# Kernel optimization log

Measured on AMD Instinct MI355X. Metric: run time of the kernel, lower is better.

## Reference

```python
import jax, jax.numpy as jnp
import numpy as np

B, S, D = 8, 4096, 512
EPS = 1e-6


def setup_inputs() -> dict:
    key = jax.random.key(0)
    ks = jax.random.split(key, 9)
    scale = 1.0 / np.sqrt(D)
    inp = {
        "x_seq": jax.random.normal(ks[0], (B, S, D), dtype=jnp.float32),
        "Wq": jax.random.uniform(ks[1], (D, D), jnp.float32, -scale, scale),
        "bq": jax.random.uniform(ks[2], (D,), jnp.float32, -scale, scale),
        "Wk": jax.random.uniform(ks[3], (D, D), jnp.float32, -scale, scale),
        "bk": jax.random.uniform(ks[4], (D,), jnp.float32, -scale, scale),
        "Wv": jax.random.uniform(ks[5], (D, D), jnp.float32, -scale, scale),
        "bv": jax.random.uniform(ks[6], (D,), jnp.float32, -scale, scale),
        "Wa": jax.random.uniform(ks[7], (D, D), jnp.float32, -scale, scale),
        "ba": jax.random.uniform(ks[8], (D,), jnp.float32, -scale, scale),
    }
    return inp


def _forward(x_seq, Wq, bq, Wk, bk, Wv, bv, Wa, ba):
    # Precompute all projections for the whole sequence (big GEMMs).
    q = jax.nn.relu(jnp.einsum('bsd,ed->bse', x_seq, Wq) + bq)  # phi = relu
    k = jax.nn.relu(jnp.einsum('bsd,ed->bse', x_seq, Wk) + bk)
    v = jnp.einsum('bsd,ed->bse', x_seq, Wv) + bv
    a = jax.nn.sigmoid(jnp.einsum('bsd,ed->bse', x_seq, Wa) + ba)

    # time-major for scan: (S, B, D)
    qs, ks_, vs, as_ = (jnp.swapaxes(t, 0, 1) for t in (q, k, v, a))

    def step(carry, inp):
        s, z = carry                      # s: (B,D,D), z: (B,D)
        q_t, k_t, v_t, a_t = inp
        s = a_t[:, :, None] * s + k_t[:, :, None] * v_t[:, None, :]
        z = a_t * z + k_t
        num = jnp.einsum('bi,bij->bj', q_t, s)
        den = jnp.sum(q_t * z, axis=-1, keepdims=True) + EPS
        return (s, z), num / den

    s0 = jnp.zeros((x_seq.shape[0], x_seq.shape[2], x_seq.shape[2]), x_seq.dtype)
    z0 = jnp.zeros((x_seq.shape[0], x_seq.shape[2]), x_seq.dtype)
    _, ys = jax.lax.scan(step, (s0, z0), (qs, ks_, vs, as_))
    return jnp.swapaxes(ys, 0, 1)  # (B, S, D)


def reference(x_seq, Wq, bq, Wk, bk, Wv, bv, Wa, ba):
    return _forward(x_seq, Wq, bq, Wk, bk, Wv, bv, Wa, ba)
```

## Files before the change

### kernel.cpp

```cpp
#include <hip/hip_runtime.h>
#include <hip/hip_bf16.h>
#include <cstdint>
#include <cstddef>

#define D_DIM 512
#define B_DIM 8
#define S_DIM 4096
#define M_DIM (B_DIM * S_DIM)
#define CHUNK 64
#define NCHUNK (S_DIM / CHUNK)
#define NSEG 8
#define CSEG (NCHUNK / NSEG)
#define EPS_C 1e-6f

typedef __attribute__((ext_vector_type(8))) short bf16x8;
typedef __attribute__((ext_vector_type(4))) float f32x4;

#define GLOAD_LDS16(src, dst)                                              \
  __builtin_amdgcn_global_load_lds(                                        \
      (const __attribute__((address_space(1))) void*)(src),                \
      (__attribute__((address_space(3))) void*)(dst), 16, 0, 0)

__device__ __forceinline__ unsigned short f2bf(float f) {
  uint32_t u = __float_as_uint(f);
  u = (u + 0x7fffu + ((u >> 16) & 1u)) >> 16;
  return (unsigned short)u;
}
__device__ __forceinline__ float bf2f(unsigned short s) { return __uint_as_float(((uint32_t)s) << 16); }

__global__ void cvt_f32_bf16(const float* __restrict__ in, unsigned short* __restrict__ out, int n4) {
  int i = blockIdx.x * blockDim.x + threadIdx.x;
  int stride = gridDim.x * blockDim.x;
  for (; i < n4; i += stride) {
    float4 f = ((const float4*)in)[i];
    ushort4 o;
    o.x = f2bf(f.x); o.y = f2bf(f.y); o.z = f2bf(f.z); o.w = f2bf(f.w);
    ((ushort4*)out)[i] = o;
  }
}

#define PTM 256
#define PTN 256
#define PBK 64

__global__ __launch_bounds__(512, 2) void proj_gemm(
    const unsigned short* __restrict__ Xb,
    const unsigned short* __restrict__ Wb,
    const float* __restrict__ bq, const float* __restrict__ bk,
    const float* __restrict__ bv, const float* __restrict__ ba,
    unsigned short* __restrict__ q_ws, unsigned short* __restrict__ k_ws,
    unsigned short* __restrict__ v_ws, unsigned short* __restrict__ g_ws) {
  __shared__ unsigned short SB[2 * (PTM + PTN) * PBK];

  const int proj = blockIdx.z;
  const unsigned short* W = Wb + (size_t)proj * D_DIM * D_DIM;
  const int m0 = blockIdx.x * PTM;
  const int n0 = blockIdx.y * PTN;
  const int lane = threadIdx.x & 63;
  const int w = threadIdx.x >> 6;
  const int l16 = lane & 15, q4 = lane >> 4;
  const int wm = (w >> 2) * 128;
  const int wn = (w & 3) * 64;

  f32x4 acc[8][4];
#pragma unroll
  for (int m = 0; m < 8; ++m)
#pragma unroll
    for (int n = 0; n < 4; ++n) acc[m][n] = (f32x4){0.f, 0.f, 0.f, 0.f};

  const int srow = lane >> 3;
  const int sg = lane & 7;

  auto STAGE = [&](int buf, int kc) {
    unsigned short* A = SB + buf * ((PTM + PTN) * PBK);
    unsigned short* Bs = A + PTM * PBK;
#pragma unroll
    for (int q = 0; q < 4; ++q) {
      const int row = w * 32 + q * 8 + srow;
      const int g = sg ^ (row & 7);
      GLOAD_LDS16(&Xb[(size_t)(m0 + row) * D_DIM + kc + g * 8], &A[(w * 32 + q * 8) * PBK]);
      GLOAD_LDS16(&W[(size_t)(n0 + row) * D_DIM + kc + g * 8], &Bs[(w * 32 + q * 8) * PBK]);
    }
  };

  STAGE(0, 0);
  __syncthreads();

  for (int t = 0; t < D_DIM / PBK; ++t) {
    const int cur = t & 1;
    if (t + 1 < D_DIM / PBK) STAGE(cur ^ 1, (t + 1) * PBK);

    const unsigned short* A = SB + cur * ((PTM + PTN) * PBK);
    const unsigned short* Bs = A + PTM * PBK;
    const int rsw = l16 & 7;
#pragma unroll
    for (int ks = 0; ks < 2; ++ks) {
      const int gphys = ((ks * 4 + q4) ^ rsw) * 8;
      bf16x8 afr[8], bfr[4];
#pragma unroll
      for (int m = 0; m < 8; ++m)
        afr[m] = *(const bf16x8*)&A[(wm + m * 16 + l16) * PBK + gphys];
#pragma unroll
      for (int n = 0; n < 4; ++n)
        bfr[n] = *(const bf16x8*)&Bs[(wn + n * 16 + l16) * PBK + gphys];
#pragma unroll
      for (int m = 0; m < 8; ++m)
#pragma unroll
        for (int n = 0; n < 4; ++n)
          acc[m][n] = __builtin_amdgcn_mfma_f32_16x16x32_bf16(afr[m], bfr[n], acc[m][n], 0, 0, 0);
    }
    __syncthreads();
  }

  const float* bias = (proj == 0) ? bq : (proj == 1) ? bk : (proj == 2) ? bv : ba;
  unsigned short* outp = (proj == 0) ? q_ws : (proj == 1) ? k_ws : (proj == 2) ? v_ws : g_ws;
  const bool do_relu = (proj <= 1);
  unsigned short* EP = &SB[w * 128 * 32];

#pragma unroll
  for (int p = 0; p < 2; ++p) {
#pragma unroll
    for (int half = 0; half < 2; ++half) {
      const int in_idx = p * 2 + half;
      const int nn = n0 + wn + in_idx * 16 + l16;
      const float bn = bias[nn];
#pragma unroll
      for (int m = 0; m < 8; ++m) {
#pragma unroll
        for (int vv = 0; vv < 4; ++vv) {
          float val = acc[m][in_idx][vv] + bn;
          if (do_relu) val = fmaxf(val, 0.f);
          EP[(m * 16 + q4 * 4 + vv) * 32 + half * 16 + l16] = f2bf(val);
        }
      }
    }
#pragma unroll
    for (int it = 0; it < 8; ++it) {
      const int row = it * 16 + (lane >> 2);
      const int ccol = (lane & 3) * 8;
      bf16x8 vdat = *(const bf16x8*)&EP[row * 32 + ccol];
      size_t gidx = (size_t)(m0 + wm + row) * D_DIM + (size_t)(n0 + wn + p * 32 + ccol);
      *(bf16x8*)&outp[gidx] = vdat;
    }
  }
}

__global__ __launch_bounds__(512) void prep(
    const unsigned short* __restrict__ q, const unsigned short* __restrict__ k,
    const unsigned short* __restrict__ g,
    unsigned short* __restrict__ qt, unsigned short* __restrict__ kt,
    unsigned short* __restrict__ kh,
    float* __restrict__ Af, float* __restrict__ khs) {
  __shared__ float segp[8][512];
  const int c = blockIdx.x, b = blockIdx.y;
  const int seg = threadIdx.x >> 6;
  const int t = threadIdx.x & 63;
  const int i0 = t * 8;
  const int r0 = seg * 8;
  const size_t t0 = (size_t)b * S_DIM + (size_t)c * CHUNK;
  const size_t cb = ((size_t)b * NCHUNK + c) * D_DIM;

  float sp[8];
#pragma unroll
  for (int j = 0; j < 8; ++j) sp[j] = 1.f;
  for (int r = 0; r < 8; ++r) {
    bf16x8 gv = *(const bf16x8*)&g[(t0 + r0 + r) * D_DIM + i0];
#pragma unroll
    for (int j = 0; j < 8; ++j)
      sp[j] *= 1.f / (1.f + __expf(-bf2f((unsigned short)gv[j])));
  }
  *(float4*)&segp[seg][i0] = *(float4*)&sp[0];
  *(float4*)&segp[seg][i0 + 4] = *(float4*)&sp[4];
  __syncthreads();

  float pre[8], tot[8];
#pragma unroll
  for (int j = 0; j < 8; ++j) { pre[j] = 1.f; tot[j] = 1.f; }
  for (int s2 = 0; s2 < 8; ++s2) {
    float4 v0 = *(const float4*)&segp[s2][i0];
    float4 v1 = *(const float4*)&segp[s2][i0 + 4];
    float v[8] = {v0.x, v0.y, v0.z, v0.w, v1.x, v1.y, v1.z, v1.w};
#pragma unroll
    for (int j = 0; j < 8; ++j) {
      tot[j] *= v[j];
      if (s2 < seg) pre[j] *= v[j];
    }
  }
  if (seg == 0) {
    float4 a0 = {tot[0], tot[1], tot[2], tot[3]};
    float4 a1 = {tot[4], tot[5], tot[6], tot[7]};
    *(float4*)&Af[cb + i0] = a0;
    *(float4*)&Af[cb + i0 + 4] = a1;
  }

  float cum[8], ssum[8];
#pragma unroll
  for (int j = 0; j < 8; ++j) { cum[j] = pre[j]; ssum[j] = 0.f; }
  for (int r = 0; r < 8; ++r) {
    size_t idx = (t0 + r0 + r) * D_DIM + i0;
    bf16x8 gv = *(const bf16x8*)&g[idx];
    bf16x8 qv8 = *(const bf16x8*)&q[idx];
    bf16x8 kv8 = *(const bf16x8*)&k[idx];
    bf16x8 oq, ok, okh;
#pragma unroll
    for (int j = 0; j < 8; ++j) {
      cum[j] *= 1.f / (1.f + __expf(-bf2f((unsigned short)gv[j])));
      float qv = bf2f((unsigned short)qv8[j]);
      float kv = bf2f((unsigned short)kv8[j]);
      oq[j] = (short)f2bf(qv * cum[j]);
      float inv = 1.f / cum[j];
      ok[j] = (short)f2bf(kv * inv);
      float khf = kv * (tot[j] * inv);
      okh[j] = (short)f2bf(khf);
      ssum[j] += khf;
    }
    *(bf16x8*)&qt[idx] = oq;
    *(bf16x8*)&kt[idx] = ok;
    *(bf16x8*)&kh[idx] = okh;
  }

  __syncthreads();
  *(float4*)&segp[seg][i0] = *(float4*)&ssum[0];
  *(float4*)&segp[seg][i0 + 4] = *(float4*)&ssum[4];
  __syncthreads();
  if (seg == 0) {
    float s[8];
#pragma unroll
    for (int j = 0; j < 8; ++j) s[j] = 0.f;
    for (int s2 = 0; s2 < 8; ++s2) {
      float4 v0 = *(const float4*)&segp[s2][i0];
      float4 v1 = *(const float4*)&segp[s2][i0 + 4];
      s[0] += v0.x; s[1] += v0.y; s[2] += v0.z; s[3] += v0.w;
      s[4] += v1.x; s[5] += v1.y; s[6] += v1.z; s[7] += v1.w;
    }
    float4 a0 = {s[0], s[1], s[2], s[3]};
    float4 a1 = {s[4], s[5], s[6], s[7]};
    *(float4*)&khs[cb + i0] = a0;
    *(float4*)&khs[cb + i0 + 4] = a1;
  }
}

__global__ __launch_bounds__(256) void transpose_cd(
    const unsigned short* __restrict__ in, unsigned short* __restrict__ outT) {
  __shared__ unsigned short tile[CHUNK][264];
  const int c = blockIdx.x, b = blockIdx.y;
  const size_t base_in = ((size_t)b * S_DIM + (size_t)c * CHUNK) * D_DIM;
  const size_t base_out = ((size_t)b * NCHUNK + c) * (size_t)D_DIM * CHUNK;
  const int tid = threadIdx.x;
#pragma unroll
  for (int h = 0; h < 2; ++h) {
    if (h) __syncthreads();
#pragma unroll
    for (int it = 0; it < 8; ++it) {
      int flat = (it * 256 + tid) * 8;
      int row = flat >> 8;
      int col = flat & 255;
      *(uint4*)&tile[row][col] = *(const uint4*)&in[base_in + (size_t)row * D_DIM + h * 256 + col];
    }
    __syncthreads();
#pragma unroll
    for (int it = 0; it < 8; ++it) {
      int wq = it * 256 + tid;
      int i_loc = wq >> 3;
      int r0 = (wq & 7) * 8;
      ushort4 v0, v1;
      v0.x = tile[r0 + 0][i_loc]; v0.y = tile[r0 + 1][i_loc];
      v0.z = tile[r0 + 2][i_loc]; v0.w = tile[r0 + 3][i_loc];
      v1.x = tile[r0 + 4][i_loc]; v1.y = tile[r0 + 5][i_loc];
      v1.z = tile[r0 + 6][i_loc]; v1.w = tile[r0 + 7][i_loc];
      size_t o = base_out + (size_t)(h * 256 + i_loc) * CHUNK + r0;
      *(ushort4*)&outT[o] = v0;
      *(ushort4*)&outT[o + 4] = v1;
    }
  }
}

__global__ __launch_bounds__(256) void intra(
    const unsigned short* __restrict__ qt, const unsigned short* kt,
    const unsigned short* __restrict__ VT,
    unsigned short* numI, float* __restrict__ rs) {
  __shared__ unsigned short P_lds[CHUNK][CHUNK + 8];
  const int c = blockIdx.x, b = blockIdx.y;
  const size_t t0 = (size_t)b * S_DIM + (size_t)c * CHUNK;
  const int lane = threadIdx.x & 63, w = threadIdx.x >> 6;
  const int l16 = lane & 15, q4 = lane >> 4;

  f32x4 accP[4];
#pragma unroll
  for (int n = 0; n < 4; ++n) accP[n] = (f32x4){0.f, 0.f, 0.f, 0.f};
#pragma unroll
  for (int ks = 0; ks < 16; ++ks) {
    bf16x8 afr = *(const bf16x8*)&qt[(t0 + 16 * w + l16) * D_DIM + 32 * ks + 8 * q4];
#pragma unroll
    for (int n = 0; n < 4; ++n) {
      bf16x8 bfr = *(const bf16x8*)&kt[(t0 + 16 * n + l16) * D_DIM + 32 * ks + 8 * q4];
      accP[n] = __builtin_amdgcn_mfma_f32_16x16x32_bf16(afr, bfr, accP[n], 0, 0, 0);
    }
  }
  float rsum[4] = {0.f, 0.f, 0.f, 0.f};
#pragma unroll
  for (int n = 0; n < 4; ++n) {
    int m = 16 * n + l16;
#pragma unroll
    for (int vv = 0; vv < 4; ++vv) {
      int r = 16 * w + 4 * q4 + vv;
      float pv = (m <= r) ? accP[n][vv] : 0.f;
      rsum[vv] += pv;
      P_lds[r][m] = f2bf(pv);
    }
  }
#pragma unroll
  for (int msk = 1; msk < 16; msk <<= 1) {
#pragma unroll
    for (int vv = 0; vv < 4; ++vv) rsum[vv] += __shfl_xor(rsum[vv], msk, 64);
  }
  if (l16 == 0) {
#pragma unroll
    for (int vv = 0; vv < 4; ++vv) rs[t0 + 16 * w + 4 * q4 + vv] = rsum[vv];
  }
  __syncthreads();
  bf16x8 pa0 = *(const bf16x8*)&P_lds[16 * w + l16][8 * q4];
  bf16x8 pa1 = *(const bf16x8*)&P_lds[16 * w + l16][32 + 8 * q4];
  const size_t vtb = ((size_t)b * NCHUNK + c) * (size_t)D_DIM * CHUNK;
#pragma unroll 4
  for (int nt = 0; nt < 32; ++nt) {
    bf16x8 b0 = *(const bf16x8*)&VT[vtb + (size_t)(nt * 16 + l16) * CHUNK + 8 * q4];
    bf16x8 b1 = *(const bf16x8*)&VT[vtb + (size_t)(nt * 16 + l16) * CHUNK + 32 + 8 * q4];
    f32x4 acc = (f32x4){0.f, 0.f, 0.f, 0.f};
    acc = __builtin_amdgcn_mfma_f32_16x16x32_bf16(pa0, b0, acc, 0, 0, 0);
    acc = __builtin_amdgcn_mfma_f32_16x16x32_bf16(pa1, b1, acc, 0, 0, 0);
#pragma unroll
    for (int vv = 0; vv < 4; ++vv)
      numI[(t0 + 16 * w + 4 * q4 + vv) * D_DIM + nt * 16 + l16] = f2bf(acc[vv]);
  }
}

__global__ __launch_bounds__(512) void zscan(
    const float* __restrict__ Af, const float* __restrict__ khs,
    float* __restrict__ zall, float* __restrict__ Pseg) {
  const int b = blockIdx.x;
  const int i = threadIdx.x;
  float z = 0.f, rp = 1.f;
  for (int c = 0; c < NCHUNK; ++c) {
    const size_t cb = ((size_t)b * NCHUNK + c) * D_DIM;
    zall[cb + i] = z;
    float af = Af[cb + i];
    z = fmaf(af, z, khs[cb + i]);
    rp *= af;
    if ((c & (CSEG - 1)) == CSEG - 1) {
      Pseg[((size_t)b * NSEG + (c / CSEG)) * D_DIM + i] = rp;
      rp = 1.f;
    }
  }
}

__global__ __launch_bounds__(512) void denk(
    const unsigned short* __restrict__ qt, const float* __restrict__ zall,
    float* rs_invden) {
  const int c = blockIdx.x, b = blockIdx.y;
  const int lane = threadIdx.x & 63, w = threadIdx.x >> 6;
  const size_t t0 = (size_t)b * S_DIM + (size_t)c * CHUNK;
  const size_t zb = ((size_t)b * NCHUNK + c) * D_DIM;
  float4 z0 = *(const float4*)&zall[zb + lane * 8];
  float4 z1 = *(const float4*)&zall[zb + lane * 8 + 4];
#pragma unroll
  for (int rr = 0; rr < 8; ++rr) {
    int r = 8 * w + rr;
    bf16x8 qv = *(const bf16x8*)&qt[(t0 + r) * D_DIM + lane * 8];
    float p = 0.f;
    p = fmaf(bf2f((unsigned short)qv[0]), z0.x, p);
    p = fmaf(bf2f((unsigned short)qv[1]), z0.y, p);
    p = fmaf(bf2f((unsigned short)qv[2]), z0.z, p);
    p = fmaf(bf2f((unsigned short)qv[3]), z0.w, p);
    p = fmaf(bf2f((unsigned short)qv[4]), z1.x, p);
    p = fmaf(bf2f((unsigned short)qv[5]), z1.y, p);
    p = fmaf(bf2f((unsigned short)qv[6]), z1.z, p);
    p = fmaf(bf2f((unsigned short)qv[7]), z1.w, p);
#pragma unroll
    for (int msk = 1; msk < 64; msk <<= 1) p += __shfl_xor(p, msk, 64);
    if (lane == 0) {
      float* iv = &rs_invden[t0 + r];
      *iv = 1.f / (p + *iv + EPS_C);
    }
  }
}

__global__ __launch_bounds__(512, 2) void useg_k(
    const unsigned short* __restrict__ khT, const unsigned short* __restrict__ VT,
    const float* __restrict__ Af, unsigned short* __restrict__ U) {
  __shared__ unsigned short VTl[2][128 * 64];
  const int s = blockIdx.x, jt = blockIdx.y, b = blockIdx.z;
  const int lane = threadIdx.x & 63, w = threadIdx.x >> 6;
  const int l16 = lane & 15, q4 = lane >> 4;
  const int j0 = jt * 128;
  const int iw = 64 * w;
  const int vrow = lane >> 3;
  const int vswz = (lane & 7) ^ (vrow & 7);

  f32x4 acc[4][8];
#pragma unroll
  for (int T = 0; T < 4; ++T)
#pragma unroll
    for (int h = 0; h < 8; ++h) acc[T][h] = (f32x4){0.f, 0.f, 0.f, 0.f};

  const size_t cb0 = ((size_t)b * NCHUNK + s * CSEG) * D_DIM;
  {
    const size_t ob0 = cb0 * CHUNK;
#pragma unroll
    for (int kk = 0; kk < 2; ++kk) {
      const int k = 2 * w + kk;
      GLOAD_LDS16(&VT[ob0 + (size_t)(j0 + 8 * k + vrow) * CHUNK + vswz * 8],
                  &VTl[0][k * 512]);
    }
  }
  bf16x8 a0[4], a1[4];
  {
    const size_t ob0 = cb0 * CHUNK;
#pragma unroll
    for (int T = 0; T < 4; ++T) {
      a0[T] = *(const bf16x8*)&khT[ob0 + (size_t)(iw + 16 * T + l16) * CHUNK + 8 * q4];
      a1[T] = *(const bf16x8*)&khT[ob0 + (size_t)(iw + 16 * T + l16) * CHUNK + 32 + 8 * q4];
    }
  }

  for (int cc = 0; cc < CSEG; ++cc) {
    const size_t cb = cb0 + (size_t)cc * D_DIM;
    __syncthreads();
    if (cc + 1 < CSEG) {
      const size_t obn = (cb + D_DIM) * CHUNK;
#pragma unroll
      for (int kk = 0; kk < 2; ++kk) {
        const int k = 2 * w + kk;
        GLOAD_LDS16(&VT[obn + (size_t)(j0 + 8 * k + vrow) * CHUNK + vswz * 8],
                    &VTl[(cc + 1) & 1][k * 512]);
      }
    }
#pragma unroll
    for (int T = 0; T < 4; ++T) {
      float4 af = *(const float4*)&Af[cb + iw + 16 * T + 4 * q4];
#pragma unroll
      for (int h = 0; h < 8; ++h) {
        acc[T][h][0] *= af.x; acc[T][h][1] *= af.y; acc[T][h][2] *= af.z; acc[T][h][3] *= af.w;
      }
    }
    const unsigned short* Vb = VTl[cc & 1];
#pragma unroll
    for (int h = 0; h < 8; ++h) {
      const int jpos = 16 * h + l16;
      const int swz = jpos & 7;
      bf16x8 bv0 = *(const bf16x8*)&Vb[jpos * 64 + ((q4 ^ swz) * 8)];
      bf16x8 bv1 = *(const bf16x8*)&Vb[jpos * 64 + (((4 + q4) ^ swz) * 8)];
#pragma unroll
      for (int T = 0; T < 4; ++T) {
        acc[T][h] = __builtin_amdgcn_mfma_f32_16x16x32_bf16(a0[T], bv0, acc[T][h], 0, 0, 0);
        acc[T][h] = __builtin_amdgcn_mfma_f32_16x16x32_bf16(a1[T], bv1, acc[T][h], 0, 0, 0);
      }
    }
    if (cc + 1 < CSEG) {
      const size_t obn = (cb + D_DIM) * CHUNK;
#pragma unroll
      for (int T = 0; T < 4; ++T) {
        a0[T] = *(const bf16x8*)&khT[obn + (size_t)(iw + 16 * T + l16) * CHUNK + 8 * q4];
        a1[T] = *(const bf16x8*)&khT[obn + (size_t)(iw + 16 * T + l16) * CHUNK + 32 + 8 * q4];
      }
    }
  }
  const size_t ub = ((size_t)b * NSEG + s) * D_DIM;
#pragma unroll
  for (int T = 0; T < 4; ++T)
#pragma unroll
    for (int h = 0; h < 8; ++h) {
      uint2 pk;
      pk.x = (uint32_t)f2bf(acc[T][h][0]) | ((uint32_t)f2bf(acc[T][h][1]) << 16);
      pk.y = (uint32_t)f2bf(acc[T][h][2]) | ((uint32_t)f2bf(acc[T][h][3]) << 16);
      *(uint2*)&U[(ub + j0 + 16 * h + l16) * (size_t)D_DIM + iw + 16 * T + 4 * q4] = pk;
    }
}

__global__ __launch_bounds__(256) void sscan(
    const float* __restrict__ Pseg, unsigned short* __restrict__ U) {
  const int b = blockIdx.y;
  const int flat = blockIdx.x * 256 + threadIdx.x;
  const int j = flat >> 6;
  const int i0 = (flat & 63) * 8;
  float acc[8];
#pragma unroll
  for (int t = 0; t < 8; ++t) acc[t] = 0.f;
  for (int s = 0; s < NSEG; ++s) {
    const size_t pb = ((size_t)b * NSEG + s) * D_DIM;
    unsigned short* up = &U[(pb + j) * (size_t)D_DIM + i0];
    uint4 u = *(const uint4*)up;
    float4 p0 = *(const float4*)&Pseg[pb + i0];
    float4 p1 = *(const float4*)&Pseg[pb + i0 + 4];
    float uv[8];
    uv[0] = bf2f((unsigned short)(u.x & 0xffff)); uv[1] = bf2f((unsigned short)(u.x >> 16));
    uv[2] = bf2f((unsigned short)(u.y & 0xffff)); uv[3] = bf2f((unsigned short)(u.y >> 16));
    uv[4] = bf2f((unsigned short)(u.z & 0xffff)); uv[5] = bf2f((unsigned short)(u.z >> 16));
    uv[6] = bf2f((unsigned short)(u.w & 0xffff)); uv[7] = bf2f((unsigned short)(u.w >> 16));
    uint4 o;
    o.x = (uint32_t)f2bf(acc[0]) | ((uint32_t)f2bf(acc[1]) << 16);
    o.y = (uint32_t)f2bf(acc[2]) | ((uint32_t)f2bf(acc[3]) << 16);
    o.z = (uint32_t)f2bf(acc[4]) | ((uint32_t)f2bf(acc[5]) << 16);
    o.w = (uint32_t)f2bf(acc[6]) | ((uint32_t)f2bf(acc[7]) << 16);
    *(uint4*)up = o;
    acc[0] = fmaf(p0.x, acc[0], uv[0]);
    acc[1] = fmaf(p0.y, acc[1], uv[1]);
    acc[2] = fmaf(p0.z, acc[2], uv[2]);
    acc[3] = fmaf(p0.w, acc[3], uv[3]);
    acc[4] = fmaf(p1.x, acc[4], uv[4]);
    acc[5] = fmaf(p1.y, acc[5], uv[5]);
    acc[6] = fmaf(p1.z, acc[6], uv[6]);
    acc[7] = fmaf(p1.w, acc[7], uv[7]);
  }
}

__global__ __launch_bounds__(512, 2) void scan2(
    const unsigned short* __restrict__ qt, const unsigned short* __restrict__ khT,
    const unsigned short* __restrict__ VT, const float* __restrict__ Af,
    const unsigned short* __restrict__ Sin,
    const unsigned short* __restrict__ numI, const float* __restrict__ invden,
    float* __restrict__ out) {
  __shared__ unsigned short STj[128][520];
  __shared__ unsigned short VTl[128 * 64];
  const int s = blockIdx.x, jt = blockIdx.y, b = blockIdx.z;
  const int lane = threadIdx.x & 63, w = threadIdx.x >> 6;
  const int l16 = lane & 15, q4 = lane >> 4;
  const int j0 = jt * 128;
  const int iw = 64 * w;
  const int rw = 16 * (w & 3);
  const int jo = 64 * (w >> 2);
  const int vrow = lane >> 3;
  const int vswz = (lane & 7) ^ (vrow & 7);

  f32x4 acc[4][8];

  {
    const size_t pb = ((size_t)b * NSEG + s) * D_DIM;
#pragma unroll
    for (int T = 0; T < 4; ++T)
#pragma unroll
      for (int h = 0; h < 8; ++h) {
        uint2 uu = *(const uint2*)&Sin[(pb + j0 + 16 * h + l16) * (size_t)D_DIM + iw + 16 * T + 4 * q4];
        acc[T][h][0] = bf2f((unsigned short)(uu.x & 0xffff));
        acc[T][h][1] = bf2f((unsigned short)(uu.x >> 16));
        acc[T][h][2] = bf2f((unsigned short)(uu.y & 0xffff));
        acc[T][h][3] = bf2f((unsigned short)(uu.y >> 16));
      }
  }

  for (int cc = 0; cc < CSEG; ++cc) {
    const int c = s * CSEG + cc;
    const size_t cb = ((size_t)b * NCHUNK + c) * D_DIM;
    const size_t t0 = (size_t)b * S_DIM + (size_t)c * CHUNK;
    const size_t ob = cb * CHUNK;
    const bool upd = (cc != CSEG - 1);

    bf16x8 a0[4], a1[4];
    if (upd) {
#pragma unroll
      for (int kk = 0; kk < 2; ++kk) {
        const int k = 2 * w + kk;
        GLOAD_LDS16(&VT[ob + (size_t)(j0 + 8 * k + vrow) * CHUNK + vswz * 8],
                    &VTl[k * 512]);
      }
#pragma unroll
      for (int T = 0; T < 4; ++T) {
        a0[T] = *(const bf16x8*)&khT[ob + (size_t)(iw + 16 * T + l16) * CHUNK + 8 * q4];
        a1[T] = *(const bf16x8*)&khT[ob + (size_t)(iw + 16 * T + l16) * CHUNK + 32 + 8 * q4];
      }
    }

#pragma unroll
    for (int T = 0; T < 4; ++T)
#pragma unroll
      for (int h = 0; h < 8; ++h) {
        uint2 pk;
        pk.x = (uint32_t)f2bf(acc[T][h][0]) | ((uint32_t)f2bf(acc[T][h][1]) << 16);
        pk.y = (uint32_t)f2bf(acc[T][h][2]) | ((uint32_t)f2bf(acc[T][h][3]) << 16);
        *(uint2*)&STj[16 * h + l16][iw + 16 * T + 4 * q4] = pk;
      }
    __syncthreads();

    {
      f32x4 accO[4];
#pragma unroll
      for (int h = 0; h < 4; ++h) accO[h] = (f32x4){0.f, 0.f, 0.f, 0.f};
#pragma unroll
      for (int ks = 0; ks < 16; ++ks) {
        bf16x8 afr = *(const bf16x8*)&qt[(t0 + rw + l16) * D_DIM + 32 * ks + 8 * q4];
#pragma unroll
        for (int h = 0; h < 4; ++h) {
          bf16x8 bfr = *(const bf16x8*)&STj[jo + 16 * h + l16][32 * ks + 8 * q4];
          accO[h] = __builtin_amdgcn_mfma_f32_16x16x32_bf16(afr, bfr, accO[h], 0, 0, 0);
        }
      }
#pragma unroll
      for (int h = 0; h < 4; ++h)
#pragma unroll
        for (int vv = 0; vv < 4; ++vv) {
          size_t t = t0 + rw + 4 * q4 + vv;
          int j = j0 + jo + 16 * h + l16;
          float idv = invden[t];
          float nI = bf2f(numI[t * D_DIM + j]);
          out[t * D_DIM + j] = (accO[h][vv] + nI) * idv;
        }
    }

    if (upd) {
#pragma unroll
      for (int T = 0; T < 4; ++T) {
        float4 af = *(const float4*)&Af[cb + iw + 16 * T + 4 * q4];
#pragma unroll
        for (int h = 0; h < 8; ++h) {
          acc[T][h][0] *= af.x; acc[T][h][1] *= af.y; acc[T][h][2] *= af.z; acc[T][h][3] *= af.w;
        }
      }
#pragma unroll
      for (int h = 0; h < 8; ++h) {
        const int jpos = 16 * h + l16;
        const int swz = jpos & 7;
        bf16x8 bv0 = *(const bf16x8*)&VTl[jpos * 64 + ((q4 ^ swz) * 8)];
        bf16x8 bv1 = *(const bf16x8*)&VTl[jpos * 64 + (((4 + q4) ^ swz) * 8)];
#pragma unroll
        for (int T = 0; T < 4; ++T) {
          acc[T][h] = __builtin_amdgcn_mfma_f32_16x16x32_bf16(a0[T], bv0, acc[T][h], 0, 0, 0);
          acc[T][h] = __builtin_amdgcn_mfma_f32_16x16x32_bf16(a1[T], bv1, acc[T][h], 0, 0, 0);
        }
      }
    }
    __syncthreads();
  }
}

extern "C" void kernel_launch(void* const* d_in, const int* in_sizes, int n_in,
                              void* d_out, int out_size, void* d_ws, size_t ws_size,
                              hipStream_t stream) {
  const float* x  = (const float*)d_in[0];
  const float* Wq = (const float*)d_in[1];
  const float* bq = (const float*)d_in[2];
  const float* Wk = (const float*)d_in[3];
  const float* bk = (const float*)d_in[4];
  const float* Wv = (const float*)d_in[5];
  const float* bv = (const float*)d_in[6];
  const float* Wa = (const float*)d_in[7];
  const float* ba = (const float*)d_in[8];
  float* out = (float*)d_out;

  const size_t MD2 = (size_t)M_DIM * D_DIM * 2;
  uint8_t* w = (uint8_t*)d_ws;
  unsigned short* xb   = (unsigned short*)w; w += MD2;
  unsigned short* wb   = (unsigned short*)w; w += (size_t)4 * D_DIM * D_DIM * 2;
  unsigned short* q_ws = (unsigned short*)w; w += MD2;
  unsigned short* k_ws = (unsigned short*)w; w += MD2;
  unsigned short* v_ws = (unsigned short*)w; w += MD2;
  unsigned short* g_ws = (unsigned short*)w; w += MD2;
  float* Af     = (float*)w; w += (size_t)B_DIM * NCHUNK * D_DIM * 4;
  float* khs    = (float*)w; w += (size_t)B_DIM * NCHUNK * D_DIM * 4;
  float* invden = (float*)w; w += (size_t)M_DIM * 4;

  unsigned short* qt   = xb;
  unsigned short* kt   = q_ws;
  unsigned short* kh   = k_ws;
  unsigned short* VT   = g_ws;
  unsigned short* khT  = v_ws;
  unsigned short* numI = q_ws;
  unsigned short* U    = k_ws;
  float* zall = (float*)wb;
  float* Pseg = (float*)((uint8_t*)wb + (1 << 20));

  cvt_f32_bf16<<<1024, 256, 0, stream>>>(x, xb, M_DIM * D_DIM / 4);
  cvt_f32_bf16<<<128, 256, 0, stream>>>(Wq, wb + 0 * D_DIM * D_DIM, D_DIM * D_DIM / 4);
  cvt_f32_bf16<<<128, 256, 0, stream>>>(Wk, wb + 1 * D_DIM * D_DIM, D_DIM * D_DIM / 4);
  cvt_f32_bf16<<<128, 256, 0, stream>>>(Wv, wb + 2 * D_DIM * D_DIM, D_DIM * D_DIM / 4);
  cvt_f32_bf16<<<128, 256, 0, stream>>>(Wa, wb + 3 * D_DIM * D_DIM, D_DIM * D_DIM / 4);

  proj_gemm<<<dim3(M_DIM / PTM, D_DIM / PTN, 4), 512, 0, stream>>>(
      xb, wb, bq, bk, bv, ba, q_ws, k_ws, v_ws, g_ws);

  prep<<<dim3(NCHUNK, B_DIM), 512, 0, stream>>>(q_ws, k_ws, g_ws, qt, kt, kh, Af, khs);
  transpose_cd<<<dim3(NCHUNK, B_DIM), 256, 0, stream>>>(v_ws, VT);
  transpose_cd<<<dim3(NCHUNK, B_DIM), 256, 0, stream>>>(kh, khT);
  zscan<<<B_DIM, 512, 0, stream>>>(Af, khs, zall, Pseg);
  intra<<<dim3(NCHUNK, B_DIM), 256, 0, stream>>>(qt, kt, VT, numI, invden);
  denk<<<dim3(NCHUNK, B_DIM), 512, 0, stream>>>(qt, zall, invden);
  useg_k<<<dim3(NSEG, 4, B_DIM), 512, 0, stream>>>(khT, VT, Af, U);
  sscan<<<dim3(128, B_DIM), 256, 0, stream>>>(Pseg, U);
  scan2<<<dim3(NSEG, 4, B_DIM), 512, 0, stream>>>(qt, khT, VT, Af, U, numI, invden, out);
}
```

Before: 508.3 us.

## Fuse denominator into intra kernel and halve j-tile in state scan kernels

Removes the separate denk kernel by computing q·z inside intra from an LDS copy of the chunk's z and combining it with the intra-chunk row sums to write invden directly. zscan is spread over 4 blocks per batch instead of one. useg_k and scan2 shrink their column tile from 128 to 64, doubling the grid to 512 blocks, halving accumulator registers and LDS, and raising the occupancy hint. The khT fragments are now loaded inside the chunk loop instead of being prefetched. Each block now reads qt/khT for a narrower output slice, so total qt and khT traffic doubles.

After: 520.4 us. 1.02x slower.

```diff
diff --git a/kernel.cpp b/kernel.cpp
--- a/kernel.cpp
+++ b/kernel.cpp
@@ -277,20 +277,31 @@
 
 __global__ __launch_bounds__(256) void intra(
     const unsigned short* __restrict__ qt, const unsigned short* kt,
-    const unsigned short* __restrict__ VT,
-    unsigned short* numI, float* __restrict__ rs) {
+    const unsigned short* __restrict__ VT, const float* __restrict__ zall,
+    unsigned short* numI, float* __restrict__ invden) {
   __shared__ unsigned short P_lds[CHUNK][CHUNK + 8];
+  __shared__ float zl[512];
+  __shared__ float rsl[64];
   const int c = blockIdx.x, b = blockIdx.y;
   const size_t t0 = (size_t)b * S_DIM + (size_t)c * CHUNK;
+  const size_t zb = ((size_t)b * NCHUNK + c) * D_DIM;
   const int lane = threadIdx.x & 63, w = threadIdx.x >> 6;
   const int l16 = lane & 15, q4 = lane >> 4;
 
+  zl[threadIdx.x] = zall[zb + threadIdx.x];
+  zl[threadIdx.x + 256] = zall[zb + threadIdx.x + 256];
+  __syncthreads();
+
   f32x4 accP[4];
 #pragma unroll
   for (int n = 0; n < 4; ++n) accP[n] = (f32x4){0.f, 0.f, 0.f, 0.f};
+  float qdotz = 0.f;
 #pragma unroll
   for (int ks = 0; ks < 16; ++ks) {
     bf16x8 afr = *(const bf16x8*)&qt[(t0 + 16 * w + l16) * D_DIM + 32 * ks + 8 * q4];
+    const float* zp = &zl[32 * ks + 8 * q4];
+#pragma unroll
+    for (int j = 0; j < 8; ++j) qdotz = fmaf(bf2f((unsigned short)afr[j]), zp[j], qdotz);
 #pragma unroll
     for (int n = 0; n < 4; ++n) {
       bf16x8 bfr = *(const bf16x8*)&kt[(t0 + 16 * n + l16) * D_DIM + 32 * ks + 8 * q4];
@@ -316,9 +327,15 @@
   }
   if (l16 == 0) {
 #pragma unroll
-    for (int vv = 0; vv < 4; ++vv) rs[t0 + 16 * w + 4 * q4 + vv] = rsum[vv];
+    for (int vv = 0; vv < 4; ++vv) rsl[16 * w + 4 * q4 + vv] = rsum[vv];
   }
   __syncthreads();
+
+  qdotz += __shfl_xor(qdotz, 16, 64);
+  qdotz += __shfl_xor(qdotz, 32, 64);
+  if (q4 == 0)
+    invden[t0 + 16 * w + l16] = 1.f / (qdotz + rsl[16 * w + l16] + EPS_C);
+
   bf16x8 pa0 = *(const bf16x8*)&P_lds[16 * w + l16][8 * q4];
   bf16x8 pa1 = *(const bf16x8*)&P_lds[16 * w + l16][32 + 8 * q4];
   const size_t vtb = ((size_t)b * NCHUNK + c) * (size_t)D_DIM * CHUNK;
@@ -335,11 +352,11 @@
   }
 }
 
-__global__ __launch_bounds__(512) void zscan(
+__global__ __launch_bounds__(128) void zscan(
     const float* __restrict__ Af, const float* __restrict__ khs,
     float* __restrict__ zall, float* __restrict__ Pseg) {
-  const int b = blockIdx.x;
-  const int i = threadIdx.x;
+  const int b = blockIdx.y;
+  const int i = blockIdx.x * 128 + threadIdx.x;
   float z = 0.f, rp = 1.f;
   for (int c = 0; c < NCHUNK; ++c) {
     const size_t cb = ((size_t)b * NCHUNK + c) * D_DIM;
@@ -354,114 +371,57 @@
   }
 }
 
-__global__ __launch_bounds__(512) void denk(
-    const unsigned short* __restrict__ qt, const float* __restrict__ zall,
-    float* rs_invden) {
-  const int c = blockIdx.x, b = blockIdx.y;
-  const int lane = threadIdx.x & 63, w = threadIdx.x >> 6;
-  const size_t t0 = (size_t)b * S_DIM + (size_t)c * CHUNK;
-  const size_t zb = ((size_t)b * NCHUNK + c) * D_DIM;
-  float4 z0 = *(const float4*)&zall[zb + lane * 8];
-  float4 z1 = *(const float4*)&zall[zb + lane * 8 + 4];
-#pragma unroll
-  for (int rr = 0; rr < 8; ++rr) {
-    int r = 8 * w + rr;
-    bf16x8 qv = *(const bf16x8*)&qt[(t0 + r) * D_DIM + lane * 8];
-    float p = 0.f;
-    p = fmaf(bf2f((unsigned short)qv[0]), z0.x, p);
-    p = fmaf(bf2f((unsigned short)qv[1]), z0.y, p);
-    p = fmaf(bf2f((unsigned short)qv[2]), z0.z, p);
-    p = fmaf(bf2f((unsigned short)qv[3]), z0.w, p);
-    p = fmaf(bf2f((unsigned short)qv[4]), z1.x, p);
-    p = fmaf(bf2f((unsigned short)qv[5]), z1.y, p);
-    p = fmaf(bf2f((unsigned short)qv[6]), z1.z, p);
-    p = fmaf(bf2f((unsigned short)qv[7]), z1.w, p);
-#pragma unroll
-    for (int msk = 1; msk < 64; msk <<= 1) p += __shfl_xor(p, msk, 64);
-    if (lane == 0) {
-      float* iv = &rs_invden[t0 + r];
-      *iv = 1.f / (p + *iv + EPS_C);
-    }
-  }
-}
-
-__global__ __launch_bounds__(512, 2) void useg_k(
+__global__ __launch_bounds__(512, 4) void useg_k(
     const unsigned short* __restrict__ khT, const unsigned short* __restrict__ VT,
     const float* __restrict__ Af, unsigned short* __restrict__ U) {
-  __shared__ unsigned short VTl[2][128 * 64];
+  __shared__ unsigned short VTl[2][64 * 64];
   const int s = blockIdx.x, jt = blockIdx.y, b = blockIdx.z;
   const int lane = threadIdx.x & 63, w = threadIdx.x >> 6;
   const int l16 = lane & 15, q4 = lane >> 4;
-  const int j0 = jt * 128;
+  const int j0 = jt * 64;
   const int iw = 64 * w;
   const int vrow = lane >> 3;
   const int vswz = (lane & 7) ^ (vrow & 7);
 
-  f32x4 acc[4][8];
+  f32x4 acc[4][4];
 #pragma unroll
   for (int T = 0; T < 4; ++T)
 #pragma unroll
-    for (int h = 0; h < 8; ++h) acc[T][h] = (f32x4){0.f, 0.f, 0.f, 0.f};
+    for (int h = 0; h < 4; ++h) acc[T][h] = (f32x4){0.f, 0.f, 0.f, 0.f};
 
   const size_t cb0 = ((size_t)b * NCHUNK + s * CSEG) * D_DIM;
-  {
-    const size_t ob0 = cb0 * CHUNK;
-#pragma unroll
-    for (int kk = 0; kk < 2; ++kk) {
-      const int k = 2 * w + kk;
-      GLOAD_LDS16(&VT[ob0 + (size_t)(j0 + 8 * k + vrow) * CHUNK + vswz * 8],
-                  &VTl[0][k * 512]);
-    }
-  }
-  bf16x8 a0[4], a1[4];
-  {
-    const size_t ob0 = cb0 * CHUNK;
-#pragma unroll
-    for (int T = 0; T < 4; ++T) {
-      a0[T] = *(const bf16x8*)&khT[ob0 + (size_t)(iw + 16 * T + l16) * CHUNK + 8 * q4];
-      a1[T] = *(const bf16x8*)&khT[ob0 + (size_t)(iw + 16 * T + l16) * CHUNK + 32 + 8 * q4];
-    }
-  }
+  GLOAD_LDS16(&VT[cb0 * CHUNK + (size_t)(j0 + 8 * w + vrow) * CHUNK + vswz * 8],
+              &VTl[0][w * 512]);
 
   for (int cc = 0; cc < CSEG; ++cc) {
     const size_t cb = cb0 + (size_t)cc * D_DIM;
+    const size_t ob = cb * CHUNK;
     __syncthreads();
     if (cc + 1 < CSEG) {
-      const size_t obn = (cb + D_DIM) * CHUNK;
-#pragma unroll
-      for (int kk = 0; kk < 2; ++kk) {
-        const int k = 2 * w + kk;
-        GLOAD_LDS16(&VT[obn + (size_t)(j0 + 8 * k + vrow) * CHUNK + vswz * 8],
-                    &VTl[(cc + 1) & 1][k * 512]);
-      }
+      GLOAD_LDS16(&VT[(cb + D_DIM) * CHUNK + (size_t)(j0 + 8 * w + vrow) * CHUNK + vswz * 8],
+                  &VTl[(cc + 1) & 1][w * 512]);
     }
 #pragma unroll
     for (int T = 0; T < 4; ++T) {
       float4 af = *(const float4*)&Af[cb + iw + 16 * T + 4 * q4];
 #pragma unroll
-      for (int h = 0; h < 8; ++h) {
+      for (int h = 0; h < 4; ++h) {
         acc[T][h][0] *= af.x; acc[T][h][1] *= af.y; acc[T][h][2] *= af.z; acc[T][h][3] *= af.w;
       }
     }
     const unsigned short* Vb = VTl[cc & 1];
 #pragma unroll
-    for (int h = 0; h < 8; ++h) {
-      const int jpos = 16 * h + l16;
-      const int swz = jpos & 7;
-      bf16x8 bv0 = *(const bf16x8*)&Vb[jpos * 64 + ((q4 ^ swz) * 8)];
-      bf16x8 bv1 = *(const bf16x8*)&Vb[jpos * 64 + (((4 + q4) ^ swz) * 8)];
-#pragma unroll
-      for (int T = 0; T < 4; ++T) {
-        acc[T][h] = __builtin_amdgcn_mfma_f32_16x16x32_bf16(a0[T], bv0, acc[T][h], 0, 0, 0);
-        acc[T][h] = __builtin_amdgcn_mfma_f32_16x16x32_bf16(a1[T], bv1, acc[T][h], 0, 0, 0);
-      }
-    }
-    if (cc + 1 < CSEG) {
-      const size_t obn = (cb + D_DIM) * CHUNK;
-#pragma unroll
-      for (int T = 0; T < 4; ++T) {
-        a0[T] = *(const bf16x8*)&khT[obn + (size_t)(iw + 16 * T + l16) * CHUNK + 8 * q4];
-        a1[T] = *(const bf16x8*)&khT[obn + (size_t)(iw + 16 * T + l16) * CHUNK + 32 + 8 * q4];
+    for (int T = 0; T < 4; ++T) {
+      bf16x8 a0 = *(const bf16x8*)&khT[ob + (size_t)(iw + 16 * T + l16) * CHUNK + 8 * q4];
+      bf16x8 a1 = *(const bf16x8*)&khT[ob + (size_t)(iw + 16 * T + l16) * CHUNK + 32 + 8 * q4];
+#pragma unroll
+      for (int h = 0; h < 4; ++h) {
+        const int jpos = 16 * h + l16;
+        const int swz = jpos & 7;
+        bf16x8 bv0 = *(const bf16x8*)&Vb[jpos * 64 + ((q4 ^ swz) * 8)];
+        bf16x8 bv1 = *(const bf16x8*)&Vb[jpos * 64 + (((4 + q4) ^ swz) * 8)];
+        acc[T][h] = __builtin_amdgcn_mfma_f32_16x16x32_bf16(a0, bv0, acc[T][h], 0, 0, 0);
+        acc[T][h] = __builtin_amdgcn_mfma_f32_16x16x32_bf16(a1, bv1, acc[T][h], 0, 0, 0);
       }
     }
   }
@@ -469,7 +429,7 @@
 #pragma unroll
   for (int T = 0; T < 4; ++T)
 #pragma unroll
-    for (int h = 0; h < 8; ++h) {
+    for (int h = 0; h < 4; ++h) {
       uint2 pk;
       pk.x = (uint32_t)f2bf(acc[T][h][0]) | ((uint32_t)f2bf(acc[T][h][1]) << 16);
       pk.y = (uint32_t)f2bf(acc[T][h][2]) | ((uint32_t)f2bf(acc[T][h][3]) << 16);
@@ -514,32 +474,32 @@
   }
 }
 
-__global__ __launch_bounds__(512, 2) void scan2(
+__global__ __launch_bounds__(512, 4) void scan2(
     const unsigned short* __restrict__ qt, const unsigned short* __restrict__ khT,
     const unsigned short* __restrict__ VT, const float* __restrict__ Af,
     const unsigned short* __restrict__ Sin,
     const unsigned short* __restrict__ numI, const float* __restrict__ invden,
     float* __restrict__ out) {
-  __shared__ unsigned short STj[128][520];
-  __shared__ unsigned short VTl[128 * 64];
+  __shared__ unsigned short STj[64][520];
+  __shared__ unsigned short VTl[64 * 64];
   const int s = blockIdx.x, jt = blockIdx.y, b = blockIdx.z;
   const int lane = threadIdx.x & 63, w = threadIdx.x >> 6;
   const int l16 = lane & 15, q4 = lane >> 4;
-  const int j0 = jt * 128;
+  const int j0 = jt * 64;
   const int iw = 64 * w;
   const int rw = 16 * (w & 3);
-  const int jo = 64 * (w >> 2);
+  const int jo = 32 * (w >> 2);
   const int vrow = lane >> 3;
   const int vswz = (lane & 7) ^ (vrow & 7);
 
-  f32x4 acc[4][8];
+  f32x4 acc[4][4];
 
   {
     const size_t pb = ((size_t)b * NSEG + s) * D_DIM;
 #pragma unroll
     for (int T = 0; T < 4; ++T)
 #pragma unroll
-      for (int h = 0; h < 8; ++h) {
+      for (int h = 0; h < 4; ++h) {
         uint2 uu = *(const uint2*)&Sin[(pb + j0 + 16 * h + l16) * (size_t)D_DIM + iw + 16 * T + 4 * q4];
         acc[T][h][0] = bf2f((unsigned short)(uu.x & 0xffff));
         acc[T][h][1] = bf2f((unsigned short)(uu.x >> 16));
@@ -555,25 +515,14 @@
     const size_t ob = cb * CHUNK;
     const bool upd = (cc != CSEG - 1);
 
-    bf16x8 a0[4], a1[4];
-    if (upd) {
-#pragma unroll
-      for (int kk = 0; kk < 2; ++kk) {
-        const int k = 2 * w + kk;
-        GLOAD_LDS16(&VT[ob + (size_t)(j0 + 8 * k + vrow) * CHUNK + vswz * 8],
-                    &VTl[k * 512]);
-      }
-#pragma unroll
-      for (int T = 0; T < 4; ++T) {
-        a0[T] = *(const bf16x8*)&khT[ob + (size_t)(iw + 16 * T + l16) * CHUNK + 8 * q4];
-        a1[T] = *(const bf16x8*)&khT[ob + (size_t)(iw + 16 * T + l16) * CHUNK + 32 + 8 * q4];
-      }
-    }
+    if (upd)
+      GLOAD_LDS16(&VT[ob + (size_t)(j0 + 8 * w + vrow) * CHUNK + vswz * 8],
+                  &VTl[w * 512]);
 
 #pragma unroll
     for (int T = 0; T < 4; ++T)
 #pragma unroll
-      for (int h = 0; h < 8; ++h) {
+      for (int h = 0; h < 4; ++h) {
         uint2 pk;
         pk.x = (uint32_t)f2bf(acc[T][h][0]) | ((uint32_t)f2bf(acc[T][h][1]) << 16);
         pk.y = (uint32_t)f2bf(acc[T][h][2]) | ((uint32_t)f2bf(acc[T][h][3]) << 16);
@@ -582,20 +531,20 @@
     __syncthreads();
 
     {
-      f32x4 accO[4];
-#pragma unroll
-      for (int h = 0; h < 4; ++h) accO[h] = (f32x4){0.f, 0.f, 0.f, 0.f};
+      f32x4 accO[2];
+#pragma unroll
+      for (int h = 0; h < 2; ++h) accO[h] = (f32x4){0.f, 0.f, 0.f, 0.f};
 #pragma unroll
       for (int ks = 0; ks < 16; ++ks) {
         bf16x8 afr = *(const bf16x8*)&qt[(t0 + rw + l16) * D_DIM + 32 * ks + 8 * q4];
 #pragma unroll
-        for (int h = 0; h < 4; ++h) {
+        for (int h = 0; h < 2; ++h) {
           bf16x8 bfr = *(const bf16x8*)&STj[jo + 16 * h + l16][32 * ks + 8 * q4];
           accO[h] = __builtin_amdgcn_mfma_f32_16x16x32_bf16(afr, bfr, accO[h], 0, 0, 0);
         }
       }
 #pragma unroll
-      for (int h = 0; h < 4; ++h)
+      for (int h = 0; h < 2; ++h)
 #pragma unroll
         for (int vv = 0; vv < 4; ++vv) {
           size_t t = t0 + rw + 4 * q4 + vv;
@@ -611,20 +560,22 @@
       for (int T = 0; T < 4; ++T) {
         float4 af = *(const float4*)&Af[cb + iw + 16 * T + 4 * q4];
 #pragma unroll
-        for (int h = 0; h < 8; ++h) {
+        for (int h = 0; h < 4; ++h) {
           acc[T][h][0] *= af.x; acc[T][h][1] *= af.y; acc[T][h][2] *= af.z; acc[T][h][3] *= af.w;
         }
       }
 #pragma unroll
-      for (int h = 0; h < 8; ++h) {
-        const int jpos = 16 * h + l16;
-        const int swz = jpos & 7;
-        bf16x8 bv0 = *(const bf16x8*)&VTl[jpos * 64 + ((q4 ^ swz) * 8)];
-        bf16x8 bv1 = *(const bf16x8*)&VTl[jpos * 64 + (((4 + q4) ^ swz) * 8)];
-#pragma unroll
-        for (int T = 0; T < 4; ++T) {
-          acc[T][h] = __builtin_amdgcn_mfma_f32_16x16x32_bf16(a0[T], bv0, acc[T][h], 0, 0, 0);
-          acc[T][h] = __builtin_amdgcn_mfma_f32_16x16x32_bf16(a1[T], bv1, acc[T][h], 0, 0, 0);
+      for (int T = 0; T < 4; ++T) {
+        bf16x8 a0 = *(const bf16x8*)&khT[ob + (size_t)(iw + 16 * T + l16) * CHUNK + 8 * q4];
+        bf16x8 a1 = *(const bf16x8*)&khT[ob + (size_t)(iw + 16 * T + l16) * CHUNK + 32 + 8 * q4];
+#pragma unroll
+        for (int h = 0; h < 4; ++h) {
+          const int jpos = 16 * h + l16;
+          const int swz = jpos & 7;
+          bf16x8 bv0 = *(const bf16x8*)&VTl[jpos * 64 + ((q4 ^ swz) * 8)];
+          bf16x8 bv1 = *(const bf16x8*)&VTl[jpos * 64 + (((4 + q4) ^ swz) * 8)];
+          acc[T][h] = __builtin_amdgcn_mfma_f32_16x16x32_bf16(a0, bv0, acc[T][h], 0, 0, 0);
+          acc[T][h] = __builtin_amdgcn_mfma_f32_16x16x32_bf16(a1, bv1, acc[T][h], 0, 0, 0);
         }
       }
     }
@@ -680,10 +631,9 @@
   prep<<<dim3(NCHUNK, B_DIM), 512, 0, stream>>>(q_ws, k_ws, g_ws, qt, kt, kh, Af, khs);
   transpose_cd<<<dim3(NCHUNK, B_DIM), 256, 0, stream>>>(v_ws, VT);
   transpose_cd<<<dim3(NCHUNK, B_DIM), 256, 0, stream>>>(kh, khT);
-  zscan<<<B_DIM, 512, 0, stream>>>(Af, khs, zall, Pseg);
-  intra<<<dim3(NCHUNK, B_DIM), 256, 0, stream>>>(qt, kt, VT, numI, invden);
-  denk<<<dim3(NCHUNK, B_DIM), 512, 0, stream>>>(qt, zall, invden);
-  useg_k<<<dim3(NSEG, 4, B_DIM), 512, 0, stream>>>(khT, VT, Af, U);
+  zscan<<<dim3(4, B_DIM), 128, 0, stream>>>(Af, khs, zall, Pseg);
+  intra<<<dim3(NCHUNK, B_DIM), 256, 0, stream>>>(qt, kt, VT, zall, numI, invden);
+  useg_k<<<dim3(NSEG, 8, B_DIM), 512, 0, stream>>>(khT, VT, Af, U);
   sscan<<<dim3(128, B_DIM), 256, 0, stream>>>(Pseg, U);
-  scan2<<<dim3(NSEG, 4, B_DIM), 512, 0, stream>>>(qt, khT, VT, Af, U, numI, invden, out);
-}
+  scan2<<<dim3(NSEG, 8, B_DIM), 512, 0, stream>>>(qt, khT, VT, Af, U, numI, invden, out);
+}
```
